# Performance work log

Hardware: AMD Instinct MI355X
Metric: run time of the kernel (lower is better)

## Reference

```python
import jax, jax.numpy as jnp
import numpy as np

N = 100000
E = 1600000
IN_C, HID_C, OUT_C = 64, 64, 32


def setup_inputs() -> dict:
    key = jax.random.key(0)
    ks = jax.random.split(key, 8)
    x = jax.random.normal(ks[0], (N, IN_C), dtype=jnp.float32)
    edge_index = jax.random.randint(ks[1], (2, E), 0, N, dtype=jnp.int64)
    # GCNConv weights (glorot-ish scale) and biases
    W1 = jax.random.normal(ks[2], (IN_C, HID_C), dtype=jnp.float32) / np.sqrt(IN_C)
    b1 = jnp.zeros((HID_C,), dtype=jnp.float32)
    W2 = jax.random.normal(ks[3], (HID_C, HID_C), dtype=jnp.float32) / np.sqrt(HID_C)
    b2 = jnp.zeros((HID_C,), dtype=jnp.float32)
    Wlin = jax.random.normal(ks[4], (HID_C, OUT_C), dtype=jnp.float32) / np.sqrt(HID_C)
    blin = jnp.zeros((OUT_C,), dtype=jnp.float32)
    return {"x": x, "edge_index": edge_index, "W1": W1, "b1": b1,
            "W2": W2, "b2": b2, "Wlin": Wlin, "blin": blin}


def _gcn_norm(edge_index):
    # PyG GCNConv default: add self-loops, symmetric normalization.
    loop = jnp.arange(N, dtype=edge_index.dtype)
    row = jnp.concatenate([edge_index[0], loop])  # source nodes [E+N]
    col = jnp.concatenate([edge_index[1], loop])  # target nodes [E+N]
    deg = jax.ops.segment_sum(jnp.ones_like(col, dtype=jnp.float32), col,
                              num_segments=N)
    dinv = jnp.where(deg > 0, deg ** -0.5, 0.0)
    norm = dinv[row] * dinv[col]  # [E+N]
    return row, col, norm


def _gcn_conv(h, W, b, row, col, norm):
    h = h @ W                                  # [N, F_out]
    msg = h[row] * norm[:, None]               # gather + scale, [E+N, F_out]
    out = jax.ops.segment_sum(msg, col, num_segments=N)  # scatter-add
    return out + b


def reference(x, edge_index, W1, b1, W2, b2, Wlin, blin):
    row, col, norm = _gcn_norm(edge_index)
    h = jax.nn.relu(_gcn_conv(x, W1, b1, row, col, norm))
    h = jax.nn.relu(_gcn_conv(h, W2, b2, row, col, norm))
    return h @ Wlin + blin
```

## Files before the change

kernel.cpp:

```cpp
#include <hip/hip_runtime.h>
#include <hip/hip_fp16.h>

#define IN_C 64
#define HID_C 64
#define OUT_C 32
#define S_NODES  512
#define S_CAP  12288
#define CHUNK_E 2048

typedef _Float16 f16_t;
typedef f16_t f16x2 __attribute__((ext_vector_type(2)));

__device__ __forceinline__ float dot2(unsigned int a, unsigned int b, float c) {
#if __has_builtin(__builtin_amdgcn_fdot2)
    return __builtin_amdgcn_fdot2(*(f16x2*)&a, *(f16x2*)&b, c, false);
#else
    float2 af = __half22float2(*(__half2*)&a);
    float2 bf = __half22float2(*(__half2*)&b);
    return fmaf(af.x, bf.x, fmaf(af.y, bf.y, c));
#endif
}

__device__ __forceinline__ int ld_edge(const void* ei, int idx, int is64) {
    if (is64) return (int)((const long long*)ei)[idx];
    return ((const int*)ei)[idx];
}

__global__ __launch_bounds__(256) void fat(const void* ei, int E,
                                           int* bcur, int NB,
                                           int* __restrict__ staging,
                                           int NEB, int GB,
                                           const float* __restrict__ x,
                                           const float* __restrict__ W1,
                                           float* __restrict__ t32, int n,
                                           const float* __restrict__ W2,
                                           const float* __restrict__ Wlin,
                                           unsigned short* __restrict__ Wh2,
                                           unsigned short* __restrict__ Whl) {
    __shared__ __align__(16) int smem[3073];
    int tid = threadIdx.x;
    int b = blockIdx.x;
    if (b < NEB) {
        int* cnt = smem;          int* boff = smem + 256;
        int* lcur = smem + 512;   int* gbase = smem + 768;
        int* stg = smem + 1024;
        int* ps64 = smem + 3072;
        if (tid == 0) *ps64 = 1;
        cnt[tid] = 0;
        __syncthreads();
        if (2 * tid + 1 < 2 * E && ((const int*)ei)[2 * tid + 1] != 0) *ps64 = 0;
        __syncthreads();
        int is64 = *ps64;
        int e0 = b * CHUNK_E;
        int e1 = min(E, e0 + CHUNK_E);
        for (int e = e0 + tid; e < e1; e += 256) {
            int dst = ld_edge(ei, E + e, is64);
            atomicAdd(&cnt[dst >> 9], 1);
        }
        __syncthreads();
        int v = cnt[tid];
        gbase[tid] = v;
        __syncthreads();
        for (int o = 1; o < 256; o <<= 1) {
            int u = (tid >= o) ? gbase[tid - o] : 0;
            __syncthreads();
            gbase[tid] += u;
            __syncthreads();
        }
        boff[tid] = gbase[tid] - v;
        lcur[tid] = boff[tid];
        __syncthreads();
        for (int e = e0 + tid; e < e1; e += 256) {
            int src = ld_edge(ei, e, is64);
            int dst = ld_edge(ei, E + e, is64);
            int p = atomicAdd(&lcur[dst >> 9], 1);
            stg[p] = src | ((dst & 511) << 17);
        }
        __syncthreads();
        if (tid < NB && cnt[tid] > 0) gbase[tid] = atomicAdd(&bcur[tid], cnt[tid]);
        __syncthreads();
        int sw = tid >> 4, sl = tid & 15;
        for (int bk = sw; bk < NB; bk += 16) {
            int c = cnt[bk];
            if (c == 0) continue;
            int o = boff[bk], g = gbase[bk];
            size_t gb = (size_t)bk * S_CAP;
            for (int j = sl; j < c; j += 16) {
                if (g + j < S_CAP) staging[gb + g + j] = stg[o + j];
            }
        }
    } else if (b < NEB + GB) {
        uint4* sA = (uint4*)smem;
        int bb = b - NEB;
        int lane = tid & 63, wave = tid >> 6;
        unsigned int wu[32];
#pragma unroll
        for (int k = 0; k < 32; k++) {
            f16x2 p;
            p.x = (f16_t)W1[(2 * k) * 64 + lane];
            p.y = (f16_t)W1[(2 * k + 1) * 64 + lane];
            wu[k] = *(unsigned int*)&p;
        }
        int base = bb * 32;
        const float2* A2 = (const float2*)x;
        int lim = n * 32;
        for (int i = tid; i < 1024; i += 256) {
            int gi = base * 32 + i;
            float2 v = (gi < lim) ? A2[gi] : make_float2(0.f, 0.f);
            ((__half2*)sA)[i] = __floats2half2_rn(v.x, v.y);
        }
        __syncthreads();
        int r0 = base + wave * 8;
        int r1 = min(r0 + 8, n);
        for (int r = r0; r < r1; r++) {
            int rr = r - base;
            float a0 = 0.f, a1 = 0.f;
#pragma unroll
            for (int j = 0; j < 8; j++) {
                uint4 u = sA[rr * 8 + j];
                a0 = dot2(u.x, wu[4 * j], a0);
                a1 = dot2(u.y, wu[4 * j + 1], a1);
                a0 = dot2(u.z, wu[4 * j + 2], a0);
                a1 = dot2(u.w, wu[4 * j + 3], a1);
            }
            t32[(size_t)r * 64 + lane] = a0 + a1;
        }
    } else {
        for (int i = tid; i < 4096; i += 256) {
            int r = i >> 6, c = i & 63;
            f16_t h2 = (f16_t)W2[r * 64 + c];
            Wh2[c * 64 + r] = *(unsigned short*)&h2;
        }
        for (int i = tid; i < 2048; i += 256) {
            int r = i >> 5, c = i & 31;
            f16_t h = (f16_t)Wlin[r * 32 + c];
            Whl[c * 64 + r] = *(unsigned short*)&h;
        }
    }
}

__global__ __launch_bounds__(256) void place_fine(const int* __restrict__ staging,
                                                  const int* __restrict__ bcur,
                                                  int* __restrict__ offs,
                                                  float* __restrict__ dinv,
                                                  int* __restrict__ rec,
                                                  const float* __restrict__ t32,
                                                  unsigned short* __restrict__ t16,
                                                  int N, int NB) {
    __shared__ int sdeg[S_NODES];
    __shared__ int tsum[256];
    __shared__ int curs[S_NODES];
    __shared__ int sb[256];
    __shared__ float sdinv[S_NODES];
    int tid = threadIdx.x;
    int vcnt = (tid < NB) ? min(bcur[tid], S_CAP) : 0;
    sb[tid] = vcnt;
    sdeg[tid] = 0;
    sdeg[tid + 256] = 0;
    __syncthreads();
    for (int o = 1; o < 256; o <<= 1) {
        int u = (tid >= o) ? sb[tid - o] : 0;
        __syncthreads();
        sb[tid] += u;
        __syncthreads();
    }
    int cnt = min(bcur[blockIdx.x], S_CAP);
    int bbase = sb[blockIdx.x] - cnt;
    if (blockIdx.x == NB - 1 && tid == 0) offs[N] = sb[255];
    int base = blockIdx.x * S_NODES;
    int nn = min(S_NODES, N - base);
    size_t sbase = (size_t)blockIdx.x * S_CAP;
    for (int j = tid; j < cnt; j += 256) atomicAdd(&sdeg[staging[sbase + j] >> 17], 1);
    __syncthreads();
    int d0 = sdeg[2 * tid], d1 = sdeg[2 * tid + 1];
    tsum[tid] = d0 + d1;
    __syncthreads();
    for (int o = 1; o < 256; o <<= 1) {
        int v = (tid >= o) ? tsum[tid - o] : 0;
        __syncthreads();
        tsum[tid] += v;
        __syncthreads();
    }
    int pre = bbase + ((tid == 0) ? 0 : tsum[tid - 1]);
    curs[2 * tid] = pre;
    curs[2 * tid + 1] = pre + d0;
    float dv0 = rsqrtf((float)(d0 + 1));
    float dv1 = rsqrtf((float)(d1 + 1));
    sdinv[2 * tid] = dv0;
    sdinv[2 * tid + 1] = dv1;
    if (2 * tid < nn) {
        offs[base + 2 * tid] = pre;
        dinv[base + 2 * tid] = dv0;
    }
    if (2 * tid + 1 < nn) {
        offs[base + 2 * tid + 1] = pre + d0;
        dinv[base + 2 * tid + 1] = dv1;
    }
    __syncthreads();
    for (int j = tid; j < cnt; j += 256) {
        int pk = staging[sbase + j];
        int p = atomicAdd(&curs[pk >> 17], 1);
        rec[p] = pk & 0x1FFFF;
    }
    const float4* tin = (const float4*)t32 + (size_t)base * 16;
    uint2* tout = (uint2*)t16 + (size_t)base * 16;
    int jmax = nn * 16;
    for (int j = tid; j < jmax; j += 256) {
        float4 v = tin[j];
        float w = sdinv[j >> 4];
        __half2 h0 = __floats2half2_rn(v.x * w, v.y * w);
        __half2 h1 = __floats2half2_rn(v.z * w, v.w * w);
        tout[j] = make_uint2(*(unsigned int*)&h0, *(unsigned int*)&h1);
    }
}

__device__ __forceinline__ void agg_consume(const uint4& v, float w, float s[8]) {
    float2 f0 = __half22float2(*(__half2*)&v.x);
    float2 f1 = __half22float2(*(__half2*)&v.y);
    float2 f2 = __half22float2(*(__half2*)&v.z);
    float2 f3 = __half22float2(*(__half2*)&v.w);
    s[0] = fmaf(f0.x, w, s[0]);
    s[1] = fmaf(f0.y, w, s[1]);
    s[2] = fmaf(f1.x, w, s[2]);
    s[3] = fmaf(f1.y, w, s[3]);
    s[4] = fmaf(f2.x, w, s[4]);
    s[5] = fmaf(f2.y, w, s[5]);
    s[6] = fmaf(f3.x, w, s[6]);
    s[7] = fmaf(f3.y, w, s[7]);
}

template <int NU>
__device__ __forceinline__ void agg_chunk(const uint4* __restrict__ t4,
                                          const int* __restrict__ rec,
                                          int beg, int node, int m, int i,
                                          int g, int gl, float s[8]) {
    int srcs[NU];
    float ws[NU];
    uint4 vs[NU];
#pragma unroll
    for (int u = 0; u < NU; u++) {
        int it = i + u * 8 + g;
        srcs[u] = (it == 0) ? node : ((it < m) ? rec[beg + it - 1] : node);
        ws[u] = (it < m) ? 1.f : 0.f;
    }
#pragma unroll
    for (int u = 0; u < NU; u++) vs[u] = t4[(size_t)srcs[u] * 8 + gl];
#pragma unroll
    for (int u = 0; u < NU; u++) agg_consume(vs[u], ws[u], s);
}

__global__ void aggregate(const unsigned short* __restrict__ t,
                          const int* __restrict__ offs, const int* __restrict__ rec,
                          const float* __restrict__ dinv, const float* __restrict__ bias,
                          unsigned short* __restrict__ acc, int n) {
    int wave = (blockIdx.x * blockDim.x + threadIdx.x) >> 6;
    int lane = threadIdx.x & 63;
    if (wave >= n) return;
    int g = lane >> 3;
    int gl = lane & 7;
    int beg = offs[wave], end = offs[wave + 1];
    int m = end - beg + 1;
    const uint4* t4 = (const uint4*)t;
    float s[8] = {0.f, 0.f, 0.f, 0.f, 0.f, 0.f, 0.f, 0.f};
    int i = 0;
    for (; m - i > 24; i += 32) agg_chunk<4>(t4, rec, beg, wave, m, i, g, gl, s);
    int rem = m - i;
    if (rem > 16)     agg_chunk<3>(t4, rec, beg, wave, m, i, g, gl, s);
    else if (rem > 8) agg_chunk<2>(t4, rec, beg, wave, m, i, g, gl, s);
    else if (rem > 0) agg_chunk<1>(t4, rec, beg, wave, m, i, g, gl, s);
#pragma unroll
    for (int k = 0; k < 8; k++) {
        s[k] += __shfl_xor(s[k], 8);
        s[k] += __shfl_xor(s[k], 16);
        s[k] += __shfl_xor(s[k], 32);
    }
    if (g == 0) {
        float d = dinv[wave];
        const float4* b4 = (const float4*)bias;
        float4 bb0 = b4[gl * 2], bb1 = b4[gl * 2 + 1];
        float o0 = fmaxf(fmaf(s[0], d, bb0.x), 0.f);
        float o1 = fmaxf(fmaf(s[1], d, bb0.y), 0.f);
        float o2 = fmaxf(fmaf(s[2], d, bb0.z), 0.f);
        float o3 = fmaxf(fmaf(s[3], d, bb0.w), 0.f);
        float o4 = fmaxf(fmaf(s[4], d, bb1.x), 0.f);
        float o5 = fmaxf(fmaf(s[5], d, bb1.y), 0.f);
        float o6 = fmaxf(fmaf(s[6], d, bb1.z), 0.f);
        float o7 = fmaxf(fmaf(s[7], d, bb1.w), 0.f);
        __half2 p0 = __floats2half2_rn(o0, o1);
        __half2 p1 = __floats2half2_rn(o2, o3);
        __half2 p2 = __floats2half2_rn(o4, o5);
        __half2 p3 = __floats2half2_rn(o6, o7);
        ((uint4*)acc)[(size_t)wave * 8 + gl] =
            make_uint4(*(unsigned int*)&p0, *(unsigned int*)&p1,
                       *(unsigned int*)&p2, *(unsigned int*)&p3);
    }
}

__global__ __launch_bounds__(256) void gemm64(const unsigned short* __restrict__ in,
                                              const unsigned short* __restrict__ Wh,
                                              unsigned short* __restrict__ out,
                                              const float* __restrict__ dinv, int n) {
    __shared__ uint4 sA[32 * 8];
    int tid = threadIdx.x;
    int lane = tid & 63, wave = tid >> 6;
    unsigned int wu[32];
    {
        const uint4* col = (const uint4*)(Wh + (size_t)lane * 64);
#pragma unroll
        for (int j = 0; j < 8; j++) {
            uint4 w4 = col[j];
            wu[4 * j] = w4.x; wu[4 * j + 1] = w4.y;
            wu[4 * j + 2] = w4.z; wu[4 * j + 3] = w4.w;
        }
    }
    int base = blockIdx.x * 32;
    const uint2* A2 = (const uint2*)in;
    int lim = n * 16;
    for (int i = tid; i < 512; i += 256) {
        int gi = base * 16 + i;
        ((uint2*)sA)[i] = (gi < lim) ? A2[gi] : make_uint2(0u, 0u);
    }
    __syncthreads();
    int r0 = base + wave * 8;
    int r1 = min(r0 + 8, n);
    for (int r = r0; r < r1; r++) {
        int rr = r - base;
        float a0 = 0.f, a1 = 0.f;
#pragma unroll
        for (int j = 0; j < 8; j++) {
            uint4 u = sA[rr * 8 + j];
            a0 = dot2(u.x, wu[4 * j], a0);
            a1 = dot2(u.y, wu[4 * j + 1], a1);
            a0 = dot2(u.z, wu[4 * j + 2], a0);
            a1 = dot2(u.w, wu[4 * j + 3], a1);
        }
        __half hv = __float2half_rn((a0 + a1) * dinv[r]);
        out[(size_t)r * 64 + lane] = *(unsigned short*)&hv;
    }
}

__global__ __launch_bounds__(256) void gemm32(const unsigned short* __restrict__ in,
                                              const unsigned short* __restrict__ Wh,
                                              const float* __restrict__ b,
                                              float* __restrict__ out, int n) {
    __shared__ uint4 sA[32 * 8];
    int tid = threadIdx.x;
    int lane = tid & 63, wave = tid >> 6;
    int c = lane & 31;
    unsigned int wu[32];
    {
        const uint4* col = (const uint4*)(Wh + (size_t)c * 64);
#pragma unroll
        for (int j = 0; j < 8; j++) {
            uint4 w4 = col[j];
            wu[4 * j] = w4.x; wu[4 * j + 1] = w4.y;
            wu[4 * j + 2] = w4.z; wu[4 * j + 3] = w4.w;
        }
    }
    float bl = b[c];
    int base = blockIdx.x * 32;
    const uint2* A2 = (const uint2*)in;
    int lim = n * 16;
    for (int i = tid; i < 512; i += 256) {
        int gi = base * 16 + i;
        ((uint2*)sA)[i] = (gi < lim) ? A2[gi] : make_uint2(0u, 0u);
    }
    __syncthreads();
    int r0 = base + wave * 8;
    int r1 = min(r0 + 8, n);
    for (int r = r0; r < r1; r++) {
        int rr = r - base;
        float a0 = 0.f, a1 = 0.f;
#pragma unroll
        for (int j = 0; j < 8; j++) {
            uint4 u = sA[rr * 8 + j];
            a0 = dot2(u.x, wu[4 * j], a0);
            a1 = dot2(u.y, wu[4 * j + 1], a1);
            a0 = dot2(u.z, wu[4 * j + 2], a0);
            a1 = dot2(u.w, wu[4 * j + 3], a1);
        }
        if (lane < 32) out[(size_t)r * 32 + c] = bl + a0 + a1;
    }
}

extern "C" void kernel_launch(void* const* d_in, const int* in_sizes, int n_in,
                              void* d_out, int out_size, void* d_ws, size_t ws_size,
                              hipStream_t stream) {
    (void)n_in; (void)out_size; (void)ws_size;
    const float* x    = (const float*)d_in[0];
    const void*  ei   = d_in[1];
    const float* W1   = (const float*)d_in[2];
    const float* b1   = (const float*)d_in[3];
    const float* W2   = (const float*)d_in[4];
    const float* b2   = (const float*)d_in[5];
    const float* Wlin = (const float*)d_in[6];
    const float* blin = (const float*)d_in[7];
    float* out = (float*)d_out;

    const int N = in_sizes[0] / IN_C;
    const int E = in_sizes[1] / 2;
    const int NB = (N + S_NODES - 1) / S_NODES;
    const int NEB = (E + CHUNK_E - 1) / CHUNK_E;
    const int GB = (N + 31) / 32;

    char* ws = (char*)d_ws;
    size_t off = 0;
    auto alloc = [&](size_t bytes) -> void* {
        size_t a = (off + 255) & ~(size_t)255;
        off = a + bytes;
        return (void*)(ws + a);
    };
    int*   offs    = (int*)  alloc((size_t)(N + 1) * 4);
    float* dinv    = (float*)alloc((size_t)N * 4);
    int*   bcur    = (int*)  alloc((size_t)NB * 4);
    int*   rec     = (int*)  alloc((size_t)E * 4);
    int*   staging = (int*)  alloc((size_t)NB * S_CAP * 4);
    float* t32     = (float*)alloc((size_t)N * HID_C * 4);
    unsigned short* t16 = (unsigned short*)alloc((size_t)N * HID_C * 2);
    unsigned short* Wh2 = (unsigned short*)alloc(64 * 64 * 2);
    unsigned short* Whl = (unsigned short*)alloc(64 * 32 * 2);
    unsigned short* acc = (unsigned short*)t32;

    hipMemsetAsync(bcur, 0, (size_t)NB * 4, stream);

    fat<<<NEB + GB + 1, 256, 0, stream>>>(ei, E, bcur, NB, staging, NEB, GB,
                                          x, W1, t32, N, W2, Wlin, Wh2, Whl);
    place_fine<<<NB, 256, 0, stream>>>(staging, bcur, offs, dinv, rec,
                                       t32, t16, N, NB);

    aggregate<<<(N + 3) / 4, 256, 0, stream>>>(t16, offs, rec, dinv, b1, acc, N);
    gemm64<<<GB, 256, 0, stream>>>(acc, Wh2, t16, dinv, N);
    aggregate<<<(N + 3) / 4, 256, 0, stream>>>(t16, offs, rec, dinv, b2, acc, N);
    gemm32<<<GB, 256, 0, stream>>>(acc, Whl, blin, out, N);
}
```

Baseline: 265.9 us.

## Use wave-shuffle scans and register-buffered edges in edge bucketing

Replaces the shared-memory Hillis-Steele block scans, which need a barrier per step, with wave-level shuffle scans plus a small cross-wave fixup in both the bucketing and placement kernels. The bucketing blocks now read each edge once into registers (16 per thread) and reuse them for the scatter pass instead of reloading them from global memory. The edge chunk per block is doubled, so fewer bucketing blocks each do more work, at the cost of more registers and shared memory. int64 edges are now read as the low 32-bit word directly.

```diff
diff --git a/kernel.cpp b/kernel.cpp
--- a/kernel.cpp
+++ b/kernel.cpp
@@ -6,7 +6,7 @@
 #define OUT_C 32
 #define S_NODES  512
 #define S_CAP  12288
-#define CHUNK_E 2048
+#define CHUNK_E 4096
 
 typedef _Float16 f16_t;
 typedef f16_t f16x2 __attribute__((ext_vector_type(2)));
@@ -21,9 +21,13 @@
 #endif
 }
 
-__device__ __forceinline__ int ld_edge(const void* ei, int idx, int is64) {
-    if (is64) return (int)((const long long*)ei)[idx];
-    return ((const int*)ei)[idx];
+__device__ __forceinline__ int wave_iscan(int x, int lane) {
+#pragma unroll
+    for (int o = 1; o < 64; o <<= 1) {
+        int y = __shfl_up(x, o);
+        if (lane >= o) x += y;
+    }
+    return x;
 }
 
 __global__ __launch_bounds__(256) void fat(const void* ei, int E,
@@ -37,14 +41,16 @@
                                            const float* __restrict__ Wlin,
                                            unsigned short* __restrict__ Wh2,
                                            unsigned short* __restrict__ Whl) {
-    __shared__ __align__(16) int smem[3073];
+    __shared__ __align__(16) int smem[5128];
     int tid = threadIdx.x;
     int b = blockIdx.x;
     if (b < NEB) {
         int* cnt = smem;          int* boff = smem + 256;
         int* lcur = smem + 512;   int* gbase = smem + 768;
         int* stg = smem + 1024;
-        int* ps64 = smem + 3072;
+        int* ps64 = smem + 5120;
+        int* wsum = smem + 5121;
+        int lane = tid & 63, wv = tid >> 6;
         if (tid == 0) *ps64 = 1;
         cnt[tid] = 0;
         __syncthreads();
@@ -53,28 +59,54 @@
         int is64 = *ps64;
         int e0 = b * CHUNK_E;
         int e1 = min(E, e0 + CHUNK_E);
-        for (int e = e0 + tid; e < e1; e += 256) {
-            int dst = ld_edge(ei, E + e, is64);
-            atomicAdd(&cnt[dst >> 9], 1);
+        const int* ei32 = (const int*)ei;
+        int rbuf[16];
+        int bbuf[16];
+        if (is64) {
+#pragma unroll
+            for (int k = 0; k < 16; k++) {
+                int e = e0 + (k << 8) + tid;
+                if (e < e1) {
+                    int src = ei32[2 * e];
+                    int dst = ei32[2 * (E + e)];
+                    rbuf[k] = src | ((dst & 511) << 17);
+                    int bk = dst >> 9;
+                    bbuf[k] = bk;
+                    atomicAdd(&cnt[bk], 1);
+                } else bbuf[k] = -1;
+            }
+        } else {
+#pragma unroll
+            for (int k = 0; k < 16; k++) {
+                int e = e0 + (k << 8) + tid;
+                if (e < e1) {
+                    int src = ei32[e];
+                    int dst = ei32[E + e];
+                    rbuf[k] = src | ((dst & 511) << 17);
+                    int bk = dst >> 9;
+                    bbuf[k] = bk;
+                    atomicAdd(&cnt[bk], 1);
+                } else bbuf[k] = -1;
+            }
         }
         __syncthreads();
         int v = cnt[tid];
-        gbase[tid] = v;
-        __syncthreads();
-        for (int o = 1; o < 256; o <<= 1) {
-            int u = (tid >= o) ? gbase[tid - o] : 0;
-            __syncthreads();
-            gbase[tid] += u;
-            __syncthreads();
-        }
-        boff[tid] = gbase[tid] - v;
-        lcur[tid] = boff[tid];
-        __syncthreads();
-        for (int e = e0 + tid; e < e1; e += 256) {
-            int src = ld_edge(ei, e, is64);
-            int dst = ld_edge(ei, E + e, is64);
-            int p = atomicAdd(&lcur[dst >> 9], 1);
-            stg[p] = src | ((dst & 511) << 17);
+        int xx = wave_iscan(v, lane);
+        if (lane == 63) wsum[wv] = xx;
+        __syncthreads();
+        int add = 0;
+#pragma unroll
+        for (int w = 0; w < 3; w++) add += (w < wv) ? wsum[w] : 0;
+        int bo = xx + add - v;
+        boff[tid] = bo;
+        lcur[tid] = bo;
+        __syncthreads();
+#pragma unroll
+        for (int k = 0; k < 16; k++) {
+            if (bbuf[k] >= 0) {
+                int p = atomicAdd(&lcur[bbuf[k]], 1);
+                stg[p] = rbuf[k];
+            }
         }
         __syncthreads();
         if (tid < NB && cnt[tid] > 0) gbase[tid] = atomicAdd(&bcur[tid], cnt[tid]);
@@ -148,22 +180,23 @@
                                                   unsigned short* __restrict__ t16,
                                                   int N, int NB) {
     __shared__ int sdeg[S_NODES];
-    __shared__ int tsum[256];
     __shared__ int curs[S_NODES];
     __shared__ int sb[256];
     __shared__ float sdinv[S_NODES];
+    __shared__ int wsum[4];
     int tid = threadIdx.x;
-    int vcnt = (tid < NB) ? min(bcur[tid], S_CAP) : 0;
-    sb[tid] = vcnt;
+    int lane = tid & 63, wv = tid >> 6;
+    int v = (tid < NB) ? min(bcur[tid], S_CAP) : 0;
     sdeg[tid] = 0;
     sdeg[tid + 256] = 0;
-    __syncthreads();
-    for (int o = 1; o < 256; o <<= 1) {
-        int u = (tid >= o) ? sb[tid - o] : 0;
-        __syncthreads();
-        sb[tid] += u;
-        __syncthreads();
-    }
+    int xx = wave_iscan(v, lane);
+    if (lane == 63) wsum[wv] = xx;
+    __syncthreads();
+    int add = 0;
+#pragma unroll
+    for (int w = 0; w < 3; w++) add += (w < wv) ? wsum[w] : 0;
+    sb[tid] = xx + add;
+    __syncthreads();
     int cnt = min(bcur[blockIdx.x], S_CAP);
     int bbase = sb[blockIdx.x] - cnt;
     if (blockIdx.x == NB - 1 && tid == 0) offs[N] = sb[255];
@@ -173,15 +206,14 @@
     for (int j = tid; j < cnt; j += 256) atomicAdd(&sdeg[staging[sbase + j] >> 17], 1);
     __syncthreads();
     int d0 = sdeg[2 * tid], d1 = sdeg[2 * tid + 1];
-    tsum[tid] = d0 + d1;
-    __syncthreads();
-    for (int o = 1; o < 256; o <<= 1) {
-        int v = (tid >= o) ? tsum[tid - o] : 0;
-        __syncthreads();
-        tsum[tid] += v;
-        __syncthreads();
-    }
-    int pre = bbase + ((tid == 0) ? 0 : tsum[tid - 1]);
+    int t = d0 + d1;
+    int x2 = wave_iscan(t, lane);
+    if (lane == 63) wsum[wv] = x2;
+    __syncthreads();
+    int add2 = 0;
+#pragma unroll
+    for (int w = 0; w < 3; w++) add2 += (w < wv) ? wsum[w] : 0;
+    int pre = bbase + x2 + add2 - t;
     curs[2 * tid] = pre;
     curs[2 * tid + 1] = pre + d0;
     float dv0 = rsqrtf((float)(d0 + 1));
@@ -206,10 +238,10 @@
     uint2* tout = (uint2*)t16 + (size_t)base * 16;
     int jmax = nn * 16;
     for (int j = tid; j < jmax; j += 256) {
-        float4 v = tin[j];
+        float4 vv = tin[j];
         float w = sdinv[j >> 4];
-        __half2 h0 = __floats2half2_rn(v.x * w, v.y * w);
-        __half2 h1 = __floats2half2_rn(v.z * w, v.w * w);
+        __half2 h0 = __floats2half2_rn(vv.x * w, vv.y * w);
+        __half2 h1 = __floats2half2_rn(vv.z * w, vv.w * w);
         tout[j] = make_uint2(*(unsigned int*)&h0, *(unsigned int*)&h1);
     }
 }
```

Result: faster. 259.3 us (-2.5%).
